# Performance work log

Measured on AMD Instinct MI355X. Metric: run time of the kernel, lower is better.

The kernel has to match this reference:

```python
import jax, jax.numpy as jnp
import numpy as np

DIM = 768
NUM_HEADS = 12
HEAD_DIM = DIM // NUM_HEADS
SCALE = HEAD_DIM ** -0.5


def setup_inputs() -> dict:
    key = jax.random.key(0)
    k1, k2, k3 = jax.random.split(key, 3)
    x = jax.random.normal(k1, (32, 577, DIM), dtype=jnp.float32)
    # torch nn.Linear weights are [out_features, in_features]
    W_qkv = jax.random.normal(k2, (3 * DIM, DIM), dtype=jnp.float32) * (DIM ** -0.5)
    W_proj = jax.random.normal(k3, (DIM, DIM), dtype=jnp.float32) * (DIM ** -0.5)
    b_proj = jnp.zeros((DIM,), dtype=jnp.float32)
    return {"x": x, "W_qkv": W_qkv, "W_proj": W_proj, "b_proj": b_proj}


def reference(x, W_qkv, W_proj, b_proj):
    B, N, C = x.shape
    H, D = NUM_HEADS, C // NUM_HEADS
    # qkv: [B, N, 3C] -> [3, B, H, N, D]
    qkv = (x @ W_qkv.T).reshape(B, N, 3, H, D).transpose(2, 0, 3, 1, 4)
    q, k, v = qkv[0], qkv[1], qkv[2]
    attn = jnp.einsum('bhnd,bhmd->bhnm', q, k) * SCALE
    attn = jax.nn.softmax(attn, axis=-1)
    out = jnp.einsum('bhnm,bhmd->bhnd', attn, v)  # [B, H, N, D]
    out = out.transpose(0, 2, 1, 3).reshape(B, N, C)
    return out @ W_proj.T + b_proj
```

## Files before the change

### kernel.cpp

```cpp
#include <hip/hip_runtime.h>
#include <math.h>

#define SEQ    577
#define BATCH  32
#define DIM    768
#define NHEAD  12
#define HDIM   64
#define MROWS  (BATCH * SEQ)
#define QKVN   (3 * DIM)

using half4   = __attribute__((ext_vector_type(4))) _Float16;
using half8   = __attribute__((ext_vector_type(8))) _Float16;
using floatx4 = __attribute__((ext_vector_type(4))) float;

typedef __attribute__((address_space(1))) const unsigned int GU;
typedef __attribute__((address_space(3))) unsigned int LU;

__device__ __forceinline__ void gld_lds16(const _Float16* g, _Float16* l) {
    __builtin_amdgcn_global_load_lds((const GU*)g, (LU*)l, 16, 0, 0);
}

__device__ __forceinline__ unsigned lds_addr(const void* p) {
    return (unsigned)(size_t)(LU*)p;
}

__global__ void cvt3_f32_f16(const float* __restrict__ a, _Float16* __restrict__ ao, int na4,
                             const float* __restrict__ b, _Float16* __restrict__ bo, int nb4,
                             const float* __restrict__ c, _Float16* __restrict__ co, int nc4)
{
    int i = blockIdx.x * blockDim.x + threadIdx.x;
    int stride = gridDim.x * blockDim.x;
    int total = na4 + nb4 + nc4;
    for (; i < total; i += stride) {
        const float4* src; half4* dst; int j = i;
        if (j < na4)            { src = (const float4*)a; dst = (half4*)ao; }
        else if ((j -= na4) < nb4) { src = (const float4*)b; dst = (half4*)bo; }
        else { j -= nb4;          src = (const float4*)c; dst = (half4*)co; }
        float4 v = src[j];
        half4 h;
        h[0] = (_Float16)v.x; h[1] = (_Float16)v.y;
        h[2] = (_Float16)v.z; h[3] = (_Float16)v.w;
        dst[j] = h;
    }
}

template<int OUT_HALF, int HAS_BIAS, int SCALEQ>
__global__ __launch_bounds__(256) void gemm_f16_lds(
    const _Float16* __restrict__ A, const _Float16* __restrict__ B,
    const float* __restrict__ bias, void* __restrict__ Cp,
    int M, int N, int K, int npm, int npn)
{
    __shared__ _Float16 As[2][128 * 32];
    __shared__ _Float16 Bs[2][128 * 32];

    const int GROUP = 8;
    int pid  = blockIdx.x;
    int ngrp = GROUP * npn;
    int g    = pid / ngrp;
    int fm   = g * GROUP;
    int gm   = npm - fm; if (gm > GROUP) gm = GROUP;
    int pm   = fm + (pid % ngrp) % gm;
    int pn   = (pid % ngrp) / gm;
    const int m0 = pm * 128, n0 = pn * 128;

    const int t    = threadIdx.x, lane = t & 63, wv = t >> 6;
    const int quad = lane >> 4,   ln   = lane & 15;
    const int wm   = wv >> 1,     wn   = wv & 1;

    floatx4 acc[4][4];
#pragma unroll
    for (int mt = 0; mt < 4; mt++)
#pragma unroll
        for (int nt = 0; nt < 4; nt++) acc[mt][nt] = {0.f, 0.f, 0.f, 0.f};

    const int sr = wv * 32 + (lane >> 2);
    const int sc = (lane & 3) * 8;
    int ma0 = m0 + sr;      if (ma0 > M - 1) ma0 = M - 1;
    int ma1 = m0 + sr + 16; if (ma1 > M - 1) ma1 = M - 1;
    const _Float16* Ag0 = A + (size_t)ma0 * K + sc;
    const _Float16* Ag1 = A + (size_t)ma1 * K + sc;
    const _Float16* Bg0 = B + (size_t)(n0 + sr) * K + sc;
    const _Float16* Bg1 = B + (size_t)(n0 + sr + 16) * K + sc;
    _Float16* Al0 = &As[0][sr * 32 + sc];
    _Float16* Al1 = &As[0][(sr + 16) * 32 + sc];
    _Float16* Bl0 = &Bs[0][sr * 32 + sc];
    _Float16* Bl1 = &Bs[0][(sr + 16) * 32 + sc];
    const int PHALF = 128 * 32;

    for (int k0 = 0; k0 < K; k0 += 64) {
        __syncthreads();
#pragma unroll
        for (int p = 0; p < 2; p++) {
            gld_lds16(Ag0 + k0 + p * 32, Al0 + p * PHALF);
            gld_lds16(Ag1 + k0 + p * 32, Al1 + p * PHALF);
            gld_lds16(Bg0 + k0 + p * 32, Bl0 + p * PHALF);
            gld_lds16(Bg1 + k0 + p * 32, Bl1 + p * PHALF);
        }
        __syncthreads();

#pragma unroll
        for (int p = 0; p < 2; p++) {
            half8 af[4], bf[4];
#pragma unroll
            for (int mt = 0; mt < 4; mt++)
                af[mt] = *(const half8*)&As[p][(wm * 64 + mt * 16 + ln) * 32 + quad * 8];
#pragma unroll
            for (int nt = 0; nt < 4; nt++)
                bf[nt] = *(const half8*)&Bs[p][(wn * 64 + nt * 16 + ln) * 32 + quad * 8];
#pragma unroll
            for (int mt = 0; mt < 4; mt++)
#pragma unroll
                for (int nt = 0; nt < 4; nt++)
                    acc[mt][nt] = __builtin_amdgcn_mfma_f32_16x16x32_f16(
                        af[mt], bf[nt], acc[mt][nt], 0, 0, 0);
        }
    }

    float bv[4];
    if constexpr (HAS_BIAS) {
#pragma unroll
        for (int nt = 0; nt < 4; nt++) bv[nt] = bias[n0 + wn * 64 + nt * 16 + ln];
    }
    float*    C32 = (float*)Cp;
    _Float16* C16 = (_Float16*)Cp;
#pragma unroll
    for (int mt = 0; mt < 4; mt++)
#pragma unroll
        for (int r = 0; r < 4; r++) {
            int m = m0 + wm * 64 + mt * 16 + quad * 4 + r;
            if (m < M) {
#pragma unroll
                for (int nt = 0; nt < 4; nt++) {
                    int col = n0 + wn * 64 + nt * 16 + ln;
                    float v = acc[mt][nt][r];
                    if constexpr (HAS_BIAS) v += bv[nt];
                    if constexpr (SCALEQ) { if (col < DIM) v *= 0.18033688f; }
                    if constexpr (OUT_HALF) C16[(size_t)m * N + col] = (_Float16)v;
                    else                    C32[(size_t)m * N + col] = v;
                }
            }
        }
}

__global__ __launch_bounds__(256) void attn_f16(
    const _Float16* __restrict__ qkv, _Float16* __restrict__ outp)
{
    __shared__ _Float16 Ks[2][64 * 64];
    __shared__ _Float16 Vs[2][64 * 64];

    const int t    = threadIdx.x, lane = t & 63, wv = t >> 6;
    const int quad = lane >> 4,   ln   = lane & 15;
    const int q0   = blockIdx.x * 128;
    const int hd   = blockIdx.y,  b    = blockIdx.z;
    const _Float16* base = qkv + (size_t)b * SEQ * QKVN;

    half8 qreg[2][2];
#pragma unroll
    for (int qc = 0; qc < 2; qc++) {
        int q = q0 + wv * 32 + qc * 16 + ln; if (q >= SEQ) q = SEQ - 1;
#pragma unroll
        for (int kd = 0; kd < 2; kd++)
            qreg[qc][kd] = *(const half8*)(base + (size_t)q * QKVN + hd * HDIM + kd * 32 + quad * 8);
    }

    const int krow = t >> 3;
    const int kdc  = (t & 7) ^ (krow & 7);
    const int vkey = ((t >> 7) << 4) + (((t >> 3) & 3) << 2) + ((t >> 1) & 3);
    const int vd0  = (((t >> 5) & 3) << 4) + ((t & 1) << 3);
    const _Float16* kcst = base + DIM     + hd * HDIM + kdc * 8;
    const _Float16* vcst = base + 2 * DIM + hd * HDIM + vd0;

    float lr[2] = {0.f, 0.f};
    floatx4 o[2][4];
#pragma unroll
    for (int qc = 0; qc < 2; qc++)
#pragma unroll
        for (int dt = 0; dt < 4; dt++) o[qc][dt] = {0.f, 0.f, 0.f, 0.f};

    const unsigned vb0 = lds_addr(&Vs[0][0]) + lane * 8;

    gld_lds16(kcst + (size_t)krow * QKVN,        &Ks[0][t * 8]);
    gld_lds16(kcst + (size_t)(krow + 32) * QKVN, &Ks[0][(t + 256) * 8]);
    gld_lds16(vcst + (size_t)vkey * QKVN,        &Vs[0][t * 8]);
    gld_lds16(vcst + (size_t)(vkey + 32) * QKVN, &Vs[0][(t + 256) * 8]);

    for (int kt0 = 0; kt0 < 10; kt0++) {
        const int cur = kt0 & 1;
        const int k0  = kt0 * 64;

        __syncthreads();

        if (kt0 < 9) {
            const int k1 = k0 + 64, nb = cur ^ 1;
            int r0 = k1 + krow;      if (r0 > SEQ - 1) r0 = SEQ - 1;
            int r1 = k1 + krow + 32; if (r1 > SEQ - 1) r1 = SEQ - 1;
            int s0 = k1 + vkey;      if (s0 > SEQ - 1) s0 = SEQ - 1;
            int s1 = k1 + vkey + 32; if (s1 > SEQ - 1) s1 = SEQ - 1;
            gld_lds16(kcst + (size_t)r0 * QKVN, &Ks[nb][t * 8]);
            gld_lds16(kcst + (size_t)r1 * QKVN, &Ks[nb][(t + 256) * 8]);
            gld_lds16(vcst + (size_t)s0 * QKVN, &Vs[nb][t * 8]);
            gld_lds16(vcst + (size_t)s1 * QKVN, &Vs[nb][(t + 256) * 8]);
        }
        __builtin_amdgcn_sched_barrier(0);

        floatx4 sacc[2][4];
#pragma unroll
        for (int qc = 0; qc < 2; qc++)
#pragma unroll
            for (int mt = 0; mt < 4; mt++) sacc[qc][mt] = {0.f, 0.f, 0.f, 0.f};
        const int xr = ln & 7;
#pragma unroll
        for (int kd = 0; kd < 2; kd++) {
            half8 kf[4];
#pragma unroll
            for (int mt = 0; mt < 4; mt++)
                kf[mt] = *(const half8*)&Ks[cur][(mt * 16 + ln) * 64 + (((kd * 4 + quad) ^ xr) << 3)];
#pragma unroll
            for (int mt = 0; mt < 4; mt++) {
                sacc[0][mt] = __builtin_amdgcn_mfma_f32_16x16x32_f16(kf[mt], qreg[0][kd], sacc[0][mt], 0, 0, 0);
                sacc[1][mt] = __builtin_amdgcn_mfma_f32_16x16x32_f16(kf[mt], qreg[1][kd], sacc[1][mt], 0, 0, 0);
            }
        }

        half4 vf[4][4];
        const unsigned vb = vb0 + (cur << 13);
#pragma unroll
        for (int kt = 0; kt < 4; kt++) {
            unsigned a = vb + kt * 2048;
            asm volatile("ds_read_b64_tr_b16 %0, %1 offset:0"    : "=v"(vf[kt][0]) : "v"(a));
            asm volatile("ds_read_b64_tr_b16 %0, %1 offset:512"  : "=v"(vf[kt][1]) : "v"(a));
            asm volatile("ds_read_b64_tr_b16 %0, %1 offset:1024" : "=v"(vf[kt][2]) : "v"(a));
            asm volatile("ds_read_b64_tr_b16 %0, %1 offset:1536" : "=v"(vf[kt][3]) : "v"(a));
        }

        if (k0 + 64 > SEQ) {
#pragma unroll
            for (int mt = 0; mt < 4; mt++)
#pragma unroll
                for (int r = 0; r < 4; r++)
                    if (k0 + mt * 16 + quad * 4 + r >= SEQ) {
                        sacc[0][mt][r] = -3e38f;
                        sacc[1][mt][r] = -3e38f;
                    }
        }

        half4 pf[2][4];
#pragma unroll
        for (int qc = 0; qc < 2; qc++) {
#pragma unroll
            for (int mt = 0; mt < 4; mt++)
#pragma unroll
                for (int r = 0; r < 4; r++) {
                    float p = exp2f(sacc[qc][mt][r]);
                    lr[qc] += p;
                    pf[qc][mt][r] = (_Float16)p;
                }
        }

        asm volatile("s_waitcnt lgkmcnt(0)" ::: "memory");
        __builtin_amdgcn_sched_barrier(0);
#pragma unroll
        for (int kt = 0; kt < 4; kt++) {
#pragma unroll
            for (int dt = 0; dt < 4; dt++) {
                o[0][dt] = __builtin_amdgcn_mfma_f32_16x16x16f16(vf[kt][dt], pf[0][kt], o[0][dt], 0, 0, 0);
                o[1][dt] = __builtin_amdgcn_mfma_f32_16x16x16f16(vf[kt][dt], pf[1][kt], o[1][dt], 0, 0, 0);
            }
        }
    }

#pragma unroll
    for (int qc = 0; qc < 2; qc++) {
        lr[qc] += __shfl_xor(lr[qc], 16);
        lr[qc] += __shfl_xor(lr[qc], 32);
    }

#pragma unroll
    for (int qc = 0; qc < 2; qc++) {
        int q = q0 + wv * 32 + qc * 16 + ln;
        if (q < SEQ) {
            float inv = 1.f / lr[qc];
#pragma unroll
            for (int dt = 0; dt < 4; dt++) {
                half4 hv;
                hv[0] = (_Float16)(o[qc][dt][0] * inv);
                hv[1] = (_Float16)(o[qc][dt][1] * inv);
                hv[2] = (_Float16)(o[qc][dt][2] * inv);
                hv[3] = (_Float16)(o[qc][dt][3] * inv);
                *(half4*)&outp[(size_t)(b * SEQ + q) * DIM + hd * HDIM + dt * 16 + quad * 4] = hv;
            }
        }
    }
}

extern "C" void kernel_launch(void* const* d_in, const int* in_sizes, int n_in,
                              void* d_out, int out_size, void* d_ws, size_t ws_size,
                              hipStream_t stream)
{
    const float* x     = (const float*)d_in[0];
    const float* Wqkv  = (const float*)d_in[1];
    const float* Wproj = (const float*)d_in[2];
    const float* bproj = (const float*)d_in[3];
    float* out = (float*)d_out;

    const size_t NX  = (size_t)MROWS * DIM;
    const size_t NWQ = (size_t)QKVN * DIM;
    const size_t NWP = (size_t)DIM * DIM;

    _Float16* x16    = (_Float16*)d_ws;
    _Float16* Wq16   = x16 + NX;
    _Float16* Wp16   = Wq16 + NWQ;
    _Float16* qkv16  = Wp16 + NWP;
    _Float16* attn16 = qkv16 + (size_t)MROWS * QKVN;

    cvt3_f32_f16<<<2048, 256, 0, stream>>>(x, x16, (int)(NX / 4),
                                           Wqkv, Wq16, (int)(NWQ / 4),
                                           Wproj, Wp16, (int)(NWP / 4));

    {
        int npm = (MROWS + 127) / 128, npn = QKVN / 128;
        gemm_f16_lds<1, 0, 1><<<npm * npn, 256, 0, stream>>>(
            x16, Wq16, nullptr, qkv16, MROWS, QKVN, DIM, npm, npn);
    }

    attn_f16<<<dim3((SEQ + 127) / 128, NHEAD, BATCH), 256, 0, stream>>>(qkv16, attn16);

    {
        int npm = (MROWS + 127) / 128, npn = DIM / 128;
        gemm_f16_lds<0, 1, 0><<<npm * npn, 256, 0, stream>>>(
            attn16, Wp16, bproj, out, MROWS, DIM, DIM, npm, npn);
    }
}
```

Baseline: 338.1 us.

## Double-buffer GEMM LDS tiles and XOR-swizzle LDS columns to avoid bank conflicts

The f16 GEMM now keeps two LDS stages for A and B. It prefetches the next K-tile with async global-to-LDS loads while MFMAs run on the current tile, which removes one barrier per iteration and hides global load latency. The 16-byte chunk column is also XOR-swizzled by row bits on both the load and the fragment read, to cut LDS bank conflicts. LDS use per block doubles to 64KB, which can lower how many blocks fit on a CU.

```diff
diff --git a/kernel.cpp b/kernel.cpp
--- a/kernel.cpp
+++ b/kernel.cpp
@@ -50,8 +50,8 @@
     const float* __restrict__ bias, void* __restrict__ Cp,
     int M, int N, int K, int npm, int npn)
 {
-    __shared__ _Float16 As[2][128 * 32];
-    __shared__ _Float16 Bs[2][128 * 32];
+    __shared__ _Float16 As[2][2 * 128 * 32];
+    __shared__ _Float16 Bs[2][2 * 128 * 32];
 
     const int GROUP = 8;
     int pid  = blockIdx.x;
@@ -73,40 +73,57 @@
 #pragma unroll
         for (int nt = 0; nt < 4; nt++) acc[mt][nt] = {0.f, 0.f, 0.f, 0.f};
 
-    const int sr = wv * 32 + (lane >> 2);
-    const int sc = (lane & 3) * 8;
+    const int sr  = wv * 32 + (lane >> 2);
+    const int scl = (lane & 3) * 8;
+    const int scg = ((lane & 3) ^ ((lane >> 3) & 3)) * 8;
     int ma0 = m0 + sr;      if (ma0 > M - 1) ma0 = M - 1;
     int ma1 = m0 + sr + 16; if (ma1 > M - 1) ma1 = M - 1;
-    const _Float16* Ag0 = A + (size_t)ma0 * K + sc;
-    const _Float16* Ag1 = A + (size_t)ma1 * K + sc;
-    const _Float16* Bg0 = B + (size_t)(n0 + sr) * K + sc;
-    const _Float16* Bg1 = B + (size_t)(n0 + sr + 16) * K + sc;
-    _Float16* Al0 = &As[0][sr * 32 + sc];
-    _Float16* Al1 = &As[0][(sr + 16) * 32 + sc];
-    _Float16* Bl0 = &Bs[0][sr * 32 + sc];
-    _Float16* Bl1 = &Bs[0][(sr + 16) * 32 + sc];
+    const _Float16* Ag0 = A + (size_t)ma0 * K + scg;
+    const _Float16* Ag1 = A + (size_t)ma1 * K + scg;
+    const _Float16* Bg0 = B + (size_t)(n0 + sr) * K + scg;
+    const _Float16* Bg1 = B + (size_t)(n0 + sr + 16) * K + scg;
     const int PHALF = 128 * 32;
-
-    for (int k0 = 0; k0 < K; k0 += 64) {
+    const int l0 = sr * 32 + scl;
+    const int l1 = (sr + 16) * 32 + scl;
+
+    const int nk = K >> 6;
+
+#pragma unroll
+    for (int p = 0; p < 2; p++) {
+        gld_lds16(Ag0 + p * 32, &As[0][l0 + p * PHALF]);
+        gld_lds16(Ag1 + p * 32, &As[0][l1 + p * PHALF]);
+        gld_lds16(Bg0 + p * 32, &Bs[0][l0 + p * PHALF]);
+        gld_lds16(Bg1 + p * 32, &Bs[0][l1 + p * PHALF]);
+    }
+
+    const int rq = (ln >> 1) & 3;
+
+    for (int it = 0; it < nk; it++) {
+        const int cur = it & 1;
+
         __syncthreads();
-#pragma unroll
-        for (int p = 0; p < 2; p++) {
-            gld_lds16(Ag0 + k0 + p * 32, Al0 + p * PHALF);
-            gld_lds16(Ag1 + k0 + p * 32, Al1 + p * PHALF);
-            gld_lds16(Bg0 + k0 + p * 32, Bl0 + p * PHALF);
-            gld_lds16(Bg1 + k0 + p * 32, Bl1 + p * PHALF);
-        }
-        __syncthreads();
+
+        if (it + 1 < nk) {
+            const int kn = (it + 1) << 6, nb = cur ^ 1;
+#pragma unroll
+            for (int p = 0; p < 2; p++) {
+                gld_lds16(Ag0 + kn + p * 32, &As[nb][l0 + p * PHALF]);
+                gld_lds16(Ag1 + kn + p * 32, &As[nb][l1 + p * PHALF]);
+                gld_lds16(Bg0 + kn + p * 32, &Bs[nb][l0 + p * PHALF]);
+                gld_lds16(Bg1 + kn + p * 32, &Bs[nb][l1 + p * PHALF]);
+            }
+        }
+        __builtin_amdgcn_sched_barrier(0);
 
 #pragma unroll
         for (int p = 0; p < 2; p++) {
             half8 af[4], bf[4];
 #pragma unroll
             for (int mt = 0; mt < 4; mt++)
-                af[mt] = *(const half8*)&As[p][(wm * 64 + mt * 16 + ln) * 32 + quad * 8];
+                af[mt] = *(const half8*)&As[cur][p * PHALF + (wm * 64 + mt * 16 + ln) * 32 + ((quad ^ rq) << 3)];
 #pragma unroll
             for (int nt = 0; nt < 4; nt++)
-                bf[nt] = *(const half8*)&Bs[p][(wn * 64 + nt * 16 + ln) * 32 + quad * 8];
+                bf[nt] = *(const half8*)&Bs[cur][p * PHALF + (wn * 64 + nt * 16 + ln) * 32 + ((quad ^ rq) << 3)];
 #pragma unroll
             for (int mt = 0; mt < 4; mt++)
 #pragma unroll
```

Result: no change. 344.5 us (+1.9%).

## Replace LDS-staged GEMM with direct global-to-register fragment loads and register double-buffering

Applied to the files above, without the earlier changes.

Both GEMM kernels drop shared-memory staging and the block-wide barriers. Each wave loads its MFMA A/B fragments straight from global memory into registers, double-buffered across K steps of 32. This removes LDS traffic and __syncthreads overhead. In exchange, waves that share rows re-read the same data from cache, and the global accesses are strided per row rather than tile-coalesced.

```diff
diff --git a/kernel.cpp b/kernel.cpp
--- a/kernel.cpp
+++ b/kernel.cpp
@@ -45,14 +45,11 @@
 }
 
 template<int OUT_HALF, int HAS_BIAS, int SCALEQ>
-__global__ __launch_bounds__(256) void gemm_f16_lds(
+__global__ __launch_bounds__(256) void gemm_f16_reg(
     const _Float16* __restrict__ A, const _Float16* __restrict__ B,
     const float* __restrict__ bias, void* __restrict__ Cp,
     int M, int N, int K, int npm, int npn)
 {
-    __shared__ _Float16 As[2][128 * 32];
-    __shared__ _Float16 Bs[2][128 * 32];
-
     const int GROUP = 8;
     int pid  = blockIdx.x;
     int ngrp = GROUP * npn;
@@ -73,48 +70,53 @@
 #pragma unroll
         for (int nt = 0; nt < 4; nt++) acc[mt][nt] = {0.f, 0.f, 0.f, 0.f};
 
-    const int sr = wv * 32 + (lane >> 2);
-    const int sc = (lane & 3) * 8;
-    int ma0 = m0 + sr;      if (ma0 > M - 1) ma0 = M - 1;
-    int ma1 = m0 + sr + 16; if (ma1 > M - 1) ma1 = M - 1;
-    const _Float16* Ag0 = A + (size_t)ma0 * K + sc;
-    const _Float16* Ag1 = A + (size_t)ma1 * K + sc;
-    const _Float16* Bg0 = B + (size_t)(n0 + sr) * K + sc;
-    const _Float16* Bg1 = B + (size_t)(n0 + sr + 16) * K + sc;
-    _Float16* Al0 = &As[0][sr * 32 + sc];
-    _Float16* Al1 = &As[0][(sr + 16) * 32 + sc];
-    _Float16* Bl0 = &Bs[0][sr * 32 + sc];
-    _Float16* Bl1 = &Bs[0][(sr + 16) * 32 + sc];
-    const int PHALF = 128 * 32;
-
-    for (int k0 = 0; k0 < K; k0 += 64) {
-        __syncthreads();
-#pragma unroll
-        for (int p = 0; p < 2; p++) {
-            gld_lds16(Ag0 + k0 + p * 32, Al0 + p * PHALF);
-            gld_lds16(Ag1 + k0 + p * 32, Al1 + p * PHALF);
-            gld_lds16(Bg0 + k0 + p * 32, Bl0 + p * PHALF);
-            gld_lds16(Bg1 + k0 + p * 32, Bl1 + p * PHALF);
-        }
-        __syncthreads();
-
-#pragma unroll
-        for (int p = 0; p < 2; p++) {
-            half8 af[4], bf[4];
-#pragma unroll
-            for (int mt = 0; mt < 4; mt++)
-                af[mt] = *(const half8*)&As[p][(wm * 64 + mt * 16 + ln) * 32 + quad * 8];
-#pragma unroll
-            for (int nt = 0; nt < 4; nt++)
-                bf[nt] = *(const half8*)&Bs[p][(wn * 64 + nt * 16 + ln) * 32 + quad * 8];
-#pragma unroll
-            for (int mt = 0; mt < 4; mt++)
-#pragma unroll
-                for (int nt = 0; nt < 4; nt++)
-                    acc[mt][nt] = __builtin_amdgcn_mfma_f32_16x16x32_f16(
-                        af[mt], bf[nt], acc[mt][nt], 0, 0, 0);
-        }
-    }
+    int r0 = m0 + wm * 64 +  0 + ln; if (r0 > M - 1) r0 = M - 1;
+    int r1 = m0 + wm * 64 + 16 + ln; if (r1 > M - 1) r1 = M - 1;
+    int r2 = m0 + wm * 64 + 32 + ln; if (r2 > M - 1) r2 = M - 1;
+    int r3 = m0 + wm * 64 + 48 + ln; if (r3 > M - 1) r3 = M - 1;
+    const _Float16* Ap0 = A + (size_t)r0 * K + quad * 8;
+    const _Float16* Ap1 = A + (size_t)r1 * K + quad * 8;
+    const _Float16* Ap2 = A + (size_t)r2 * K + quad * 8;
+    const _Float16* Ap3 = A + (size_t)r3 * K + quad * 8;
+    const int c0 = n0 + wn * 64;
+    const _Float16* Bp0 = B + (size_t)(c0 +  0 + ln) * K + quad * 8;
+    const _Float16* Bp1 = B + (size_t)(c0 + 16 + ln) * K + quad * 8;
+    const _Float16* Bp2 = B + (size_t)(c0 + 32 + ln) * K + quad * 8;
+    const _Float16* Bp3 = B + (size_t)(c0 + 48 + ln) * K + quad * 8;
+
+    const int nk = K >> 5;
+
+    half8 fa[2][4], fb[2][4];
+
+    fa[0][0] = *(const half8*)(Ap0); fa[0][1] = *(const half8*)(Ap1);
+    fa[0][2] = *(const half8*)(Ap2); fa[0][3] = *(const half8*)(Ap3);
+    fb[0][0] = *(const half8*)(Bp0); fb[0][1] = *(const half8*)(Bp1);
+    fb[0][2] = *(const half8*)(Bp2); fb[0][3] = *(const half8*)(Bp3);
+
+#define GSTEP(C, Nb, TT)                                                    \
+    {                                                                       \
+        const int khn = (((TT) + 1 < nk) ? (TT) + 1 : (TT)) << 5;           \
+        fa[Nb][0] = *(const half8*)(Ap0 + khn);                             \
+        fa[Nb][1] = *(const half8*)(Ap1 + khn);                             \
+        fa[Nb][2] = *(const half8*)(Ap2 + khn);                             \
+        fa[Nb][3] = *(const half8*)(Ap3 + khn);                             \
+        fb[Nb][0] = *(const half8*)(Bp0 + khn);                             \
+        fb[Nb][1] = *(const half8*)(Bp1 + khn);                             \
+        fb[Nb][2] = *(const half8*)(Bp2 + khn);                             \
+        fb[Nb][3] = *(const half8*)(Bp3 + khn);                             \
+        _Pragma("unroll")                                                   \
+        for (int mt = 0; mt < 4; mt++)                                      \
+            _Pragma("unroll")                                               \
+            for (int nt = 0; nt < 4; nt++)                                  \
+                acc[mt][nt] = __builtin_amdgcn_mfma_f32_16x16x32_f16(       \
+                    fa[C][mt], fb[C][nt], acc[mt][nt], 0, 0, 0);            \
+    }
+
+    for (int it = 0; it < nk; it += 2) {
+        GSTEP(0, 1, it);
+        GSTEP(1, 0, it + 1);
+    }
+#undef GSTEP
 
     float bv[4];
     if constexpr (HAS_BIAS) {
@@ -319,7 +321,7 @@
 
     {
         int npm = (MROWS + 127) / 128, npn = QKVN / 128;
-        gemm_f16_lds<1, 0, 1><<<npm * npn, 256, 0, stream>>>(
+        gemm_f16_reg<1, 0, 1><<<npm * npn, 256, 0, stream>>>(
             x16, Wq16, nullptr, qkv16, MROWS, QKVN, DIM, npm, npn);
     }
 
@@ -327,7 +329,7 @@
 
     {
         int npm = (MROWS + 127) / 128, npn = DIM / 128;
-        gemm_f16_lds<0, 1, 0><<<npm * npn, 256, 0, stream>>>(
+        gemm_f16_reg<0, 1, 0><<<npm * npn, 256, 0, stream>>>(
             attn16, Wp16, bproj, out, MROWS, DIM, DIM, npm, npn);
     }
 }
```

After: 547.7 us. +62.0%, slower.
